# Kernel tuning notes

Measured on AMD Instinct MI355X. Metric: run time of the kernel, lower is better.

The kernel has to match this reference:

```python
import jax, jax.numpy as jnp
import numpy as np

B, S, D = 8, 1024, 1024
H = 16
D_HEAD = D // H
RANK = 256
NC = 64
NE = 64
KC = 16  # top_k_compress
KE = 8   # top_k_expand


def setup_inputs() -> dict:
    key = jax.random.key(0)
    ks = jax.random.split(key, 9)
    rn = lambda k, sh, s=1.0: jax.random.normal(k, sh, jnp.float32) * s
    return {
        "x": rn(ks[0], (B, S, D)),
        "importance": jax.random.uniform(ks[1], (B, S), jnp.float32),
        "W_compress": rn(ks[2], (NC, D), 1.0 / np.sqrt(D)),
        "W_Q": rn(ks[3], (NE, D), 1.0 / np.sqrt(D)),
        "W_K": rn(ks[4], (NE, D), 1.0 / np.sqrt(D)),
        "W_V": rn(ks[5], (NE, D), 1.0 / np.sqrt(D)),
        "compress_neurons": rn(ks[6], (NC, D, RANK), 1.0 / np.sqrt(D)),
        "expand_pool": rn(ks[7], (NE, RANK, D), 1.0 / np.sqrt(RANK)),
        "W_O": rn(ks[8], (D, D), 1.0 / np.sqrt(D)),
    }


def _route(x, importance, W, k):
    """Per-token softmax router, importance-aggregated, top-k renormalized."""
    pref = jax.nn.softmax(jnp.einsum('bsd,nd->bsn', x, W), axis=-1)  # [B,S,n]
    w = jnp.einsum('bs,bsn->bn', importance, pref)                   # [B,n]
    w = w / (w.sum(-1, keepdims=True) + 1e-8)
    tw, ti = jax.lax.top_k(w, k)                                     # [B,k]
    tw = tw / (tw.sum(-1, keepdims=True) + 1e-8)
    return tw, ti


def reference(x, importance, W_compress, W_Q, W_K, W_V, compress_neurons, expand_pool, W_O):
    # --- GlobalRouters.get_attention_weights ---
    cw, ci = _route(x, importance, W_compress, KC)
    qw, qi = _route(x, importance, W_Q, KE)
    kw, ki = _route(x, importance, W_K, KE)
    vw, vi = _route(x, importance, W_V, KE)

    # --- NeuronCircuit.forward ---
    # gather + mix compress neurons: [B,KC,D,R] -> [B,D,R]
    shared_c = jnp.einsum('bk,bkdr->bdr', cw, compress_neurons[ci])
    h = jnp.einsum('bsd,bdr->bsr', x, shared_c)  # [B,S,R]

    eQ = jnp.einsum('bk,bkrd->brd', qw, expand_pool[qi])
    eK = jnp.einsum('bk,bkrd->brd', kw, expand_pool[ki])
    eV = jnp.einsum('bk,bkrd->brd', vw, expand_pool[vi])

    def heads(t):  # [B,S,D] -> [B,H,S,d_head]
        return t.reshape(B, S, H, D_HEAD).transpose(0, 2, 1, 3)

    Q = heads(jnp.einsum('bsr,brd->bsd', h, eQ))
    K = heads(jnp.einsum('bsr,brd->bsd', h, eK))
    V = heads(jnp.einsum('bsr,brd->bsd', h, eV))

    scale = 1.0 / np.sqrt(D_HEAD)
    scores = jnp.einsum('bhqd,bhkd->bhqk', Q, K) * scale
    causal = jnp.tril(jnp.ones((S, S), dtype=bool))
    scores = jnp.where(causal, scores, jnp.finfo(scores.dtype).min)
    attn = jax.nn.softmax(scores, axis=-1)
    out = jnp.einsum('bhqk,bhkd->bhqd', attn, V)
    out = out.transpose(0, 2, 1, 3).reshape(B, S, D)
    return jnp.einsum('bsd,ed->bse', out, W_O)  # expand_O (Linear, no bias)
```

## Files before the change

kernel.cpp:

```cpp
#include <hip/hip_runtime.h>

typedef __attribute__((ext_vector_type(8))) short short8;
typedef __attribute__((ext_vector_type(4))) short short4v;
typedef __attribute__((ext_vector_type(4))) float f32x4;
typedef unsigned short u16;
typedef unsigned int u32;

__device__ __forceinline__ float bf2f(u16 h) {
    return __uint_as_float(((u32)h) << 16);
}
__device__ __forceinline__ u16 f2bf(float f) {
    u32 u = __float_as_uint(f);
    u32 r = u + 0x7fffu + ((u >> 16) & 1u);
    return (u16)(r >> 16);
}
__device__ __forceinline__ u32 pack_bf(float a, float b) {
    return __builtin_amdgcn_perm(__float_as_uint(b), __float_as_uint(a), 0x07060302u);
}

__device__ __forceinline__ void async_copy16(const void* g, void* l) {
    __builtin_amdgcn_global_load_lds(
        (const __attribute__((address_space(1))) void*)g,
        (__attribute__((address_space(3))) void*)l, 16, 0, 0);
}

__global__ __launch_bounds__(256) void cvt_split(
    const float* __restrict__ in, u16* __restrict__ hi, u16* __restrict__ lo, int n4)
{
    int i = blockIdx.x * 256 + threadIdx.x;
    if (i >= n4) return;
    float4 v = ((const float4*)in)[i];
    short4v h, l;
    float vv[4] = {v.x, v.y, v.z, v.w};
#pragma unroll
    for (int j = 0; j < 4; j++) {
        u16 hb = f2bf(vv[j]);
        h[j] = (short)hb;
        l[j] = (short)f2bf(vv[j] - bf2f(hb));
    }
    ((short4v*)hi)[i] = h;
    ((short4v*)lo)[i] = l;
}

__global__ __launch_bounds__(256) void cvt_split_w4(
    const float* __restrict__ w0, const float* __restrict__ w1,
    const float* __restrict__ w2, const float* __restrict__ w3,
    u16* __restrict__ hi, u16* __restrict__ lo)
{
    const int r = blockIdx.x >> 6;
    const float* src = (r == 0) ? w0 : (r == 1) ? w1 : (r == 2) ? w2 : w3;
    int i = (blockIdx.x & 63) * 256 + threadIdx.x;
    float4 v = ((const float4*)src)[i];
    short4v h, l;
    float vv[4] = {v.x, v.y, v.z, v.w};
#pragma unroll
    for (int j = 0; j < 4; j++) {
        u16 hb = f2bf(vv[j]);
        h[j] = (short)hb;
        l[j] = (short)f2bf(vv[j] - bf2f(hb));
    }
    ((short4v*)(hi + (long)r * 65536))[i] = h;
    ((short4v*)(lo + (long)r * 65536))[i] = l;
}

__global__ __launch_bounds__(256) void cvt_bf(
    const float* __restrict__ in, u16* __restrict__ out, int n4)
{
    int i = blockIdx.x * 256 + threadIdx.x;
    if (i >= n4) return;
    float4 v = ((const float4*)in)[i];
    short4v h;
    h[0] = (short)f2bf(v.x); h[1] = (short)f2bf(v.y);
    h[2] = (short)f2bf(v.z); h[3] = (short)f2bf(v.w);
    ((short4v*)out)[i] = h;
}

template <typename CT>
__global__ __launch_bounds__(256) void gemm_bt(
    const u16* __restrict__ A, long lda, long bsA,
    const u16* __restrict__ Bm, long ldb, long bsB,
    CT* __restrict__ C, long ldc, long bsC, int K, float cscale)
{
    __shared__ __align__(16) u16 lsA[128 * 32];
    __shared__ __align__(16) u16 lsB[128 * 32];
    const int tid = threadIdx.x;
    const int wave = tid >> 6, lane = tid & 63;
    const int quad = lane >> 4, l15 = lane & 15;
    const int wm = wave >> 1, wn = wave & 1;
    const long m0 = (long)blockIdx.x * 128, n0 = (long)blockIdx.y * 128;
    A  += (long)blockIdx.z * bsA;
    Bm += (long)blockIdx.z * bsB;
    C  += (long)blockIdx.z * bsC;
    const int srow = lane >> 2, scol = (lane & 3) * 8;

    f32x4 acc[4][4];
#pragma unroll
    for (int i = 0; i < 4; i++)
#pragma unroll
        for (int j = 0; j < 4; j++) acc[i][j] = (f32x4){0.f, 0.f, 0.f, 0.f};

    const u16* ga0 = A + (m0 + (wave * 2 + 0) * 16 + srow) * lda + scol;
    const u16* ga1 = A + (m0 + (wave * 2 + 1) * 16 + srow) * lda + scol;
    const u16* gb0 = Bm + (n0 + (wave * 2 + 0) * 16 + srow) * ldb + scol;
    const u16* gb1 = Bm + (n0 + (wave * 2 + 1) * 16 + srow) * ldb + scol;
    u16* la0 = &lsA[(wave * 2 + 0) * 512];
    u16* la1 = &lsA[(wave * 2 + 1) * 512];
    u16* lb0 = &lsB[(wave * 2 + 0) * 512];
    u16* lb1 = &lsB[(wave * 2 + 1) * 512];

    for (int kk = 0; kk < K; kk += 32) {
        async_copy16(ga0 + kk, la0);
        async_copy16(ga1 + kk, la1);
        async_copy16(gb0 + kk, lb0);
        async_copy16(gb1 + kk, lb1);
        __syncthreads();
        short8 af[4], bf[4];
#pragma unroll
        for (int mt = 0; mt < 4; mt++)
            af[mt] = *(const short8*)&lsA[(wm * 64 + mt * 16 + l15) * 32 + quad * 8];
#pragma unroll
        for (int nt = 0; nt < 4; nt++)
            bf[nt] = *(const short8*)&lsB[(wn * 64 + nt * 16 + l15) * 32 + quad * 8];
#pragma unroll
        for (int mt = 0; mt < 4; mt++)
#pragma unroll
            for (int nt = 0; nt < 4; nt++)
                acc[mt][nt] = __builtin_amdgcn_mfma_f32_16x16x32_bf16(
                    af[mt], bf[nt], acc[mt][nt], 0, 0, 0);
        __syncthreads();
    }
#pragma unroll
    for (int mt = 0; mt < 4; mt++) {
        const long rowb = m0 + wm * 64 + mt * 16 + quad * 4;
#pragma unroll
        for (int nt = 0; nt < 4; nt++) {
            const long col = n0 + wn * 64 + nt * 16 + l15;
#pragma unroll
            for (int r = 0; r < 4; r++) {
                const float v = acc[mt][nt][r] * cscale;
                if constexpr (sizeof(CT) == 2)
                    C[(rowb + r) * ldc + col] = f2bf(v);
                else
                    C[(rowb + r) * ldc + col] = v;
            }
        }
    }
}

__global__ __launch_bounds__(256) void gemm_router(
    const u16* __restrict__ Ah, const u16* __restrict__ Al,
    const u16* __restrict__ Bh, const u16* __restrict__ Bl,
    float* __restrict__ C)
{
    __shared__ __align__(16) u16 lsA[128 * 32];
    __shared__ __align__(16) u16 lsB[128 * 32];
    const int tid = threadIdx.x;
    const int wave = tid >> 6, lane = tid & 63;
    const int quad = lane >> 4, l15 = lane & 15;
    const int wm = wave >> 1, wn = wave & 1;
    const long m0 = (long)blockIdx.x * 128, n0 = (long)blockIdx.y * 128;
    const int srow = lane >> 2, scol = (lane & 3) * 8;
    const long offA = (m0 + (wave * 2) * 16 + srow) * 1024 + scol;
    const long offB = (n0 + (wave * 2) * 16 + srow) * 1024 + scol;
    u16* la0 = &lsA[(wave * 2 + 0) * 512];
    u16* la1 = &lsA[(wave * 2 + 1) * 512];
    u16* lb0 = &lsB[(wave * 2 + 0) * 512];
    u16* lb1 = &lsB[(wave * 2 + 1) * 512];

    f32x4 acc[4][4];
#pragma unroll
    for (int i = 0; i < 4; i++)
#pragma unroll
        for (int j = 0; j < 4; j++) acc[i][j] = (f32x4){0.f, 0.f, 0.f, 0.f};

    for (int seg = 0; seg < 3; seg++) {
        const u16* A = (seg == 1) ? Al : Ah;
        const u16* B = (seg == 2) ? Bl : Bh;
        const u16* ga = A + offA;
        const u16* gb = B + offB;
        for (int kk = 0; kk < 1024; kk += 32) {
            async_copy16(ga + kk, la0);
            async_copy16(ga + 16384 + kk, la1);
            async_copy16(gb + kk, lb0);
            async_copy16(gb + 16384 + kk, lb1);
            __syncthreads();
            short8 af[4], bf[4];
#pragma unroll
            for (int mt = 0; mt < 4; mt++)
                af[mt] = *(const short8*)&lsA[(wm * 64 + mt * 16 + l15) * 32 + quad * 8];
#pragma unroll
            for (int nt = 0; nt < 4; nt++)
                bf[nt] = *(const short8*)&lsB[(wn * 64 + nt * 16 + l15) * 32 + quad * 8];
#pragma unroll
            for (int mt = 0; mt < 4; mt++)
#pragma unroll
                for (int nt = 0; nt < 4; nt++)
                    acc[mt][nt] = __builtin_amdgcn_mfma_f32_16x16x32_bf16(
                        af[mt], bf[nt], acc[mt][nt], 0, 0, 0);
            __syncthreads();
        }
    }
#pragma unroll
    for (int mt = 0; mt < 4; mt++) {
        const long rowb = m0 + wm * 64 + mt * 16 + quad * 4;
#pragma unroll
        for (int nt = 0; nt < 4; nt++) {
            const long col = n0 + wn * 64 + nt * 16 + l15;
#pragma unroll
            for (int r = 0; r < 4; r++)
                C[(rowb + r) * 256 + col] = acc[mt][nt][r];
        }
    }
}

__global__ __launch_bounds__(128) void router_agg(
    const float* __restrict__ logits, const float* __restrict__ imp,
    float* __restrict__ w_raw)
{
    __shared__ float pref[32][257];
    const int tid = threadIdx.x;
    const int tl = tid >> 2, r = tid & 3;
    const int s = blockIdx.x * 32 + tl;
    const int b = s >> 10;
    const float* lp = logits + (long)s * 256 + r * 64;
    float v[64];
#pragma unroll
    for (int i = 0; i < 16; i++) {
        float4 f = ((const float4*)lp)[i];
        v[i * 4 + 0] = f.x; v[i * 4 + 1] = f.y;
        v[i * 4 + 2] = f.z; v[i * 4 + 3] = f.w;
    }
    float mx = v[0];
#pragma unroll
    for (int i = 1; i < 64; i++) mx = fmaxf(mx, v[i]);
    float sum = 0.f;
#pragma unroll
    for (int i = 0; i < 64; i++) { v[i] = __expf(v[i] - mx); sum += v[i]; }
    const float scale = imp[s] / sum;
#pragma unroll
    for (int i = 0; i < 64; i++) pref[tl][r * 64 + i] = v[i] * scale;
    __syncthreads();
#pragma unroll
    for (int half = 0; half < 2; half++) {
        const int idx = tid + half * 128;
        const int r2 = idx >> 6, n = idx & 63;
        float acc = 0.f;
#pragma unroll 8
        for (int t = 0; t < 32; t++) acc += pref[t][r2 * 64 + n];
        atomicAdd(&w_raw[(r2 * 8 + b) * 64 + n], acc);
    }
}

__global__ void topk_kernel(const float* __restrict__ w_raw,
                            float* __restrict__ topw, int* __restrict__ topi)
{
    const int r = blockIdx.x >> 3, b = blockIdx.x & 7;
    const int lane = threadIdx.x;
    const int k = (r == 0) ? 16 : 8;
    float w = w_raw[(r * 8 + b) * 64 + lane];
    float tot = w;
    for (int o2 = 32; o2 >= 1; o2 >>= 1) tot += __shfl_xor(tot, o2);
    w = w / (tot + 1e-8f);
    __shared__ float tw[16];
    __shared__ int ti[16];
    float cur = w;
    float ssum = 0.f;
    for (int j = 0; j < k; j++) {
        float m = cur; int mi = lane;
        for (int o2 = 32; o2 >= 1; o2 >>= 1) {
            float om = __shfl_xor(m, o2); int oi = __shfl_xor(mi, o2);
            if (om > m || (om == m && oi < mi)) { m = om; mi = oi; }
        }
        if (lane == 0) { tw[j] = m; ti[j] = mi; }
        ssum += m;
        if (lane == mi) cur = -1e30f;
    }
    __syncthreads();
    if (lane < 16) {
        topw[(r * 8 + b) * 16 + lane] = (lane < k) ? tw[lane] / (ssum + 1e-8f) : 0.f;
        topi[(r * 8 + b) * 16 + lane] = (lane < k) ? ti[lane] : 0;
    }
}

__global__ __launch_bounds__(256) void gather_mix(
    const float* __restrict__ pool, const float* __restrict__ topw,
    const int* __restrict__ topi, u16* __restrict__ out,
    int I, int J, int k)
{
    __shared__ float tile[64][65];
    const int b = blockIdx.z;
    const long IJ = (long)I * J;
    const int i0 = blockIdx.x * 64, j0 = blockIdx.y * 64;
    const float* tw = topw + b * 16;
    const int* ti = topi + b * 16;
    const int tid = threadIdx.x;
    const int il = tid >> 2, jg = tid & 3;
    float acc[16];
#pragma unroll
    for (int m = 0; m < 16; m++) acc[m] = 0.f;
    for (int kk = 0; kk < k; kk++) {
        const float wgt = tw[kk];
        const long n = ti[kk];
        const float* src = pool + n * IJ + (long)(i0 + il) * J + j0 + jg * 16;
        float4 a0 = ((const float4*)src)[0];
        float4 a1 = ((const float4*)src)[1];
        float4 a2 = ((const float4*)src)[2];
        float4 a3 = ((const float4*)src)[3];
        acc[0] += wgt * a0.x;  acc[1] += wgt * a0.y;
        acc[2] += wgt * a0.z;  acc[3] += wgt * a0.w;
        acc[4] += wgt * a1.x;  acc[5] += wgt * a1.y;
        acc[6] += wgt * a1.z;  acc[7] += wgt * a1.w;
        acc[8] += wgt * a2.x;  acc[9] += wgt * a2.y;
        acc[10] += wgt * a2.z; acc[11] += wgt * a2.w;
        acc[12] += wgt * a3.x; acc[13] += wgt * a3.y;
        acc[14] += wgt * a3.z; acc[15] += wgt * a3.w;
    }
#pragma unroll
    for (int m = 0; m < 16; m++) tile[il][jg * 16 + m] = acc[m];
    __syncthreads();
    const int jl = tid >> 2, ig = tid & 3;
    short8 o0, o1;
#pragma unroll
    for (int m = 0; m < 8; m++) {
        o0[m] = (short)f2bf(tile[ig * 16 + m][jl]);
        o1[m] = (short)f2bf(tile[ig * 16 + 8 + m][jl]);
    }
    u16* dst = out + (long)b * IJ + (long)(j0 + jl) * I + i0 + ig * 16;
    *(short8*)dst = o0;
    *(short8*)(dst + 8) = o1;
}

__global__ __launch_bounds__(256, 2) void flash_attn(
    const u16* __restrict__ Qg, const u16* __restrict__ Kg,
    const u16* __restrict__ Vt, u16* __restrict__ Og)
{
    __shared__ __align__(16) u16 plds[4][32 * 72];
    const int tid = threadIdx.x;
    const int wv = tid >> 6, lane = tid & 63;
    const int quad = lane >> 4, l15 = lane & 15;
    const int gw = blockIdx.x * 4 + wv;
    const int pr = gw & 15;
    const int bh = gw >> 4;
    const int hh = bh & 15, bb = bh >> 4;
    const long SD = 1024L * 1024L;
    const u16* Qb = Qg + (long)bb * SD + hh * 64;
    const u16* Kb = Kg + (long)bb * SD + hh * 64;
    const u16* Vb = Vt + (long)bb * SD + (long)hh * 64 * 1024;
    u16* myp = plds[wv];

    for (int half = 0; half < 2; half++) {
        const int qt = half ? (31 - pr) : pr;
        const int q0 = qt * 32;

        short8 qf[2][2];
#pragma unroll
        for (int mt = 0; mt < 2; mt++)
#pragma unroll
            for (int kb = 0; kb < 2; kb++)
                qf[mt][kb] = *(const short8*)(Qb + (long)(q0 + mt * 16 + l15) * 1024 + kb * 32 + quad * 8);

        f32x4 o[2][4];
        float mrow[2] = {-3e38f, -3e38f}, lrow[2] = {0.f, 0.f};
#pragma unroll
        for (int mt = 0; mt < 2; mt++)
#pragma unroll
            for (int nt = 0; nt < 4; nt++) o[mt][nt] = (f32x4){0.f, 0.f, 0.f, 0.f};

        const int ntile = (q0 + 95) >> 6;
        short8 kf[4][2], kn[4][2];
#pragma unroll
        for (int kt = 0; kt < 4; kt++)
#pragma unroll
            for (int kb = 0; kb < 2; kb++)
                kf[kt][kb] = *(const short8*)(Kb + (long)(kt * 16 + l15) * 1024 + kb * 32 + quad * 8);

        for (int it = 0; it < ntile; it++) {
            const int k2 = it * 64;
            const bool last = (it == ntile - 1);
            f32x4 st[4][2];
#pragma unroll
            for (int kt = 0; kt < 4; kt++)
#pragma unroll
                for (int q_ = 0; q_ < 2; q_++) {
                    f32x4 z = (f32x4){0.f, 0.f, 0.f, 0.f};
                    z = __builtin_amdgcn_mfma_f32_16x16x32_bf16(kf[kt][0], qf[q_][0], z, 0, 0, 0);
                    z = __builtin_amdgcn_mfma_f32_16x16x32_bf16(kf[kt][1], qf[q_][1], z, 0, 0, 0);
                    st[kt][q_] = z;
                }
            short8 vf[4][2];
#pragma unroll
            for (int nt = 0; nt < 4; nt++)
#pragma unroll
                for (int kh = 0; kh < 2; kh++)
                    vf[nt][kh] = *(const short8*)(Vb + (long)(nt * 16 + l15) * 1024 + k2 + kh * 32 + quad * 8);
            if (it + 1 < ntile) {
#pragma unroll
                for (int kt = 0; kt < 4; kt++)
#pragma unroll
                    for (int kb = 0; kb < 2; kb++)
                        kn[kt][kb] = *(const short8*)(Kb + (long)(k2 + 64 + kt * 16 + l15) * 1024 + kb * 32 + quad * 8);
            }
            float am[2];
#pragma unroll
            for (int q_ = 0; q_ < 2; q_++) {
                if (last) {
#pragma unroll
                    for (int kt = 0; kt < 4; kt++)
#pragma unroll
                        for (int r = 0; r < 4; r++)
                            if (k2 + kt * 16 + quad * 4 + r > q0 + q_ * 16 + l15)
                                st[kt][q_][r] = -3e38f;
                }
                float cm = -3e38f;
#pragma unroll
                for (int kt = 0; kt < 4; kt++)
#pragma unroll
                    for (int r = 0; r < 4; r++) cm = fmaxf(cm, st[kt][q_][r]);
                cm = fmaxf(cm, __shfl_xor(cm, 16));
                cm = fmaxf(cm, __shfl_xor(cm, 32));
                const float mn = fmaxf(mrow[q_], cm);
                am[q_] = exp2f(mrow[q_] - mn);
                mrow[q_] = mn;
                const float moff = 0.00281502f - mn;
                float rs = 0.f;
#pragma unroll
                for (int kt = 0; kt < 4; kt++) {
                    float p0 = exp2f(st[kt][q_][0] + moff);
                    float p1 = exp2f(st[kt][q_][1] + moff);
                    float p2 = exp2f(st[kt][q_][2] + moff);
                    float p3 = exp2f(st[kt][q_][3] + moff);
                    rs += (p0 + p1) + (p2 + p3);
                    u32 w0 = pack_bf(p0, p1);
                    u32 w1 = pack_bf(p2, p3);
                    *(uint2*)&myp[(q_ * 16 + l15) * 72 + kt * 16 + quad * 4] = make_uint2(w0, w1);
                }
                rs += __shfl_xor(rs, 16);
                rs += __shfl_xor(rs, 32);
                lrow[q_] = lrow[q_] * am[q_] + rs;
            }
            float av[2][4];
#pragma unroll
            for (int mt = 0; mt < 2; mt++)
#pragma unroll
                for (int r = 0; r < 4; r++)
                    av[mt][r] = __shfl(am[mt], quad * 4 + r);
            asm volatile("s_waitcnt lgkmcnt(0)" ::: "memory");
            short8 pf0[2], pf1[2];
#pragma unroll
            for (int kh = 0; kh < 2; kh++) {
                pf0[kh] = *(const short8*)&myp[(l15) * 72 + kh * 32 + quad * 8];
                pf1[kh] = *(const short8*)&myp[(16 + l15) * 72 + kh * 32 + quad * 8];
            }
#pragma unroll
            for (int mt = 0; mt < 2; mt++)
#pragma unroll
                for (int nt = 0; nt < 4; nt++)
#pragma unroll
                    for (int r = 0; r < 4; r++) o[mt][nt][r] *= av[mt][r];
#pragma unroll
            for (int nt = 0; nt < 4; nt++)
#pragma unroll
                for (int kh = 0; kh < 2; kh++) {
                    o[0][nt] = __builtin_amdgcn_mfma_f32_16x16x32_bf16(pf0[kh], vf[nt][kh], o[0][nt], 0, 0, 0);
                    o[1][nt] = __builtin_amdgcn_mfma_f32_16x16x32_bf16(pf1[kh], vf[nt][kh], o[1][nt], 0, 0, 0);
                }
            if (it + 1 < ntile) {
#pragma unroll
                for (int kt = 0; kt < 4; kt++)
#pragma unroll
                    for (int kb = 0; kb < 2; kb++) kf[kt][kb] = kn[kt][kb];
            }
        }
#pragma unroll
        for (int mt = 0; mt < 2; mt++)
#pragma unroll
            for (int r = 0; r < 4; r++) {
                const float li = 1.0f / __shfl(lrow[mt], quad * 4 + r);
                const long row = q0 + mt * 16 + quad * 4 + r;
#pragma unroll
                for (int nt = 0; nt < 4; nt++)
                    Og[(long)bb * SD + row * 1024 + hh * 64 + nt * 16 + l15] =
                        f2bf(o[mt][nt][r] * li);
            }
    }
}

extern "C" void kernel_launch(void* const* d_in, const int* in_sizes, int n_in,
                              void* d_out, int out_size, void* d_ws, size_t ws_size,
                              hipStream_t stream)
{
    const float* x   = (const float*)d_in[0];
    const float* imp = (const float*)d_in[1];
    const float* cn  = (const float*)d_in[6];
    const float* ep  = (const float*)d_in[7];
    const float* Wo  = (const float*)d_in[8];
    float* outp = (float*)d_out;
    char* ws = (char*)d_ws;

    u16* xh = (u16*)d_out;
    u16* xl = xh + 8388608;

    u16*   Wh     = (u16*)(ws + 0);
    u16*   Wl     = (u16*)(ws + 524288);
    u16*   Wobf   = (u16*)(ws + 1048576);
    float* w_raw  = (float*)(ws + 3145728);
    float* topw   = (float*)(ws + 3153920);
    int*   topi   = (int*)(ws + 3155968);
    float* logits = (float*)(ws + 4194304);
    u16*   scT    = (u16*)(ws + 12582912);
    u16*   eQT    = (u16*)(ws + 16777216);
    u16*   Kb     = (u16*)(ws + 4194304);
    u16*   hbuf   = (u16*)(ws + 20971520);
    u16*   eKT    = (u16*)(ws + 25165824);
    u16*   eVT    = (u16*)(ws + 29360128);
    u16*   Qb     = (u16*)(ws + 33554432);
    u16*   VTb    = (u16*)(ws + 50331648);
    u16*   aout   = (u16*)(ws + 67108864);

    cvt_split<<<dim3(8192), 256, 0, stream>>>(x, xh, xl, 2097152);
    cvt_split_w4<<<dim3(256), 256, 0, stream>>>(
        (const float*)d_in[2], (const float*)d_in[3],
        (const float*)d_in[4], (const float*)d_in[5], Wh, Wl);
    cvt_bf<<<dim3(1024), 256, 0, stream>>>(Wo, Wobf, 262144);
    hipMemsetAsync(w_raw, 0, 4 * 8 * 64 * 4, stream);

    gemm_router<<<dim3(64, 2, 1), 256, 0, stream>>>(xh, xl, Wh, Wl, logits);
    router_agg<<<dim3(256), 128, 0, stream>>>(logits, imp, w_raw);
    topk_kernel<<<dim3(32), 64, 0, stream>>>(w_raw, topw, topi);
    gather_mix<<<dim3(16, 4, 8), 256, 0, stream>>>(cn, topw + 0 * 128, topi + 0 * 128, scT, 1024, 256, 16);
    gather_mix<<<dim3(4, 16, 8), 256, 0, stream>>>(ep, topw + 1 * 128, topi + 1 * 128, eQT, 256, 1024, 8);
    gather_mix<<<dim3(4, 16, 8), 256, 0, stream>>>(ep, topw + 2 * 128, topi + 2 * 128, eKT, 256, 1024, 8);
    gather_mix<<<dim3(4, 16, 8), 256, 0, stream>>>(ep, topw + 3 * 128, topi + 3 * 128, eVT, 256, 1024, 8);
    gemm_bt<u16><<<dim3(8, 2, 8), 256, 0, stream>>>(
        xh, 1024, 1048576, scT, 1024, 262144, hbuf, 256, 262144, 1024, 1.0f);
    gemm_bt<u16><<<dim3(8, 8, 8), 256, 0, stream>>>(
        hbuf, 256, 262144, eQT, 256, 262144, Qb, 1024, 1048576, 256, 0.180336880111f);
    gemm_bt<u16><<<dim3(8, 8, 8), 256, 0, stream>>>(
        hbuf, 256, 262144, eKT, 256, 262144, Kb, 1024, 1048576, 256, 1.0f);
    gemm_bt<u16><<<dim3(8, 8, 8), 256, 0, stream>>>(
        eVT, 256, 262144, hbuf, 256, 262144, VTb, 1024, 1048576, 256, 1.0f);
    flash_attn<<<dim3(512), 256, 0, stream>>>(Qb, Kb, VTb, aout);
    gemm_bt<float><<<dim3(64, 8, 1), 256, 0, stream>>>(
        aout, 1024, 0, Wobf, 1024, 0, outp, 1024, 0, 1024, 1.0f);
}
```

Measured before the change: 448.8 us.

## Split-K router and h GEMMs, batch QKV launches, shrink flash-attn tiles

The router GEMM and the x·compress GEMM are split along K, with partial results combined through float atomics into zeroed buffers. This is meant to fill more CUs, since the original grids were small. The three expand gathers and the three Q/K/V GEMMs are each merged into a single launch via blockIdx.z. Flash attention now handles 16-row query tiles per wave with no K prefetch, giving twice the blocks and a higher occupancy bound. The cost is extra memsets, atomic traffic, a separate fp32-to-bf16 conversion pass for h, and nondeterministic summation order.

```diff
diff --git a/kernel.cpp b/kernel.cpp
--- a/kernel.cpp
+++ b/kernel.cpp
@@ -147,58 +147,63 @@
     }
 }
 
-__global__ __launch_bounds__(256) void gemm_router(
-    const u16* __restrict__ Ah, const u16* __restrict__ Al,
-    const u16* __restrict__ Bh, const u16* __restrict__ Bl,
-    float* __restrict__ C)
+__global__ __launch_bounds__(256) void gemm_qkv(
+    const u16* __restrict__ hbuf, const u16* __restrict__ eQT,
+    const u16* __restrict__ eKT, const u16* __restrict__ eVT,
+    u16* __restrict__ Qb, u16* __restrict__ Kb, u16* __restrict__ VTb,
+    float qscale)
 {
     __shared__ __align__(16) u16 lsA[128 * 32];
     __shared__ __align__(16) u16 lsB[128 * 32];
+    const int mode = blockIdx.z >> 3, b = blockIdx.z & 7;
+    const long off256 = (long)b * 262144, off1k = (long)b * 1048576;
+    const u16* A  = (mode == 2) ? (eVT + off256) : (hbuf + off256);
+    const u16* Bm = (mode == 0) ? (eQT + off256) : (mode == 1) ? (eKT + off256) : (hbuf + off256);
+    u16* C = ((mode == 0) ? Qb : (mode == 1) ? Kb : VTb) + off1k;
+    const float cscale = (mode == 0) ? qscale : 1.0f;
+
     const int tid = threadIdx.x;
     const int wave = tid >> 6, lane = tid & 63;
     const int quad = lane >> 4, l15 = lane & 15;
     const int wm = wave >> 1, wn = wave & 1;
     const long m0 = (long)blockIdx.x * 128, n0 = (long)blockIdx.y * 128;
     const int srow = lane >> 2, scol = (lane & 3) * 8;
-    const long offA = (m0 + (wave * 2) * 16 + srow) * 1024 + scol;
-    const long offB = (n0 + (wave * 2) * 16 + srow) * 1024 + scol;
+
+    f32x4 acc[4][4];
+#pragma unroll
+    for (int i = 0; i < 4; i++)
+#pragma unroll
+        for (int j = 0; j < 4; j++) acc[i][j] = (f32x4){0.f, 0.f, 0.f, 0.f};
+
+    const u16* ga0 = A + (m0 + (wave * 2 + 0) * 16 + srow) * 256 + scol;
+    const u16* ga1 = A + (m0 + (wave * 2 + 1) * 16 + srow) * 256 + scol;
+    const u16* gb0 = Bm + (n0 + (wave * 2 + 0) * 16 + srow) * 256 + scol;
+    const u16* gb1 = Bm + (n0 + (wave * 2 + 1) * 16 + srow) * 256 + scol;
     u16* la0 = &lsA[(wave * 2 + 0) * 512];
     u16* la1 = &lsA[(wave * 2 + 1) * 512];
     u16* lb0 = &lsB[(wave * 2 + 0) * 512];
     u16* lb1 = &lsB[(wave * 2 + 1) * 512];
 
-    f32x4 acc[4][4];
-#pragma unroll
-    for (int i = 0; i < 4; i++)
-#pragma unroll
-        for (int j = 0; j < 4; j++) acc[i][j] = (f32x4){0.f, 0.f, 0.f, 0.f};
-
-    for (int seg = 0; seg < 3; seg++) {
-        const u16* A = (seg == 1) ? Al : Ah;
-        const u16* B = (seg == 2) ? Bl : Bh;
-        const u16* ga = A + offA;
-        const u16* gb = B + offB;
-        for (int kk = 0; kk < 1024; kk += 32) {
-            async_copy16(ga + kk, la0);
-            async_copy16(ga + 16384 + kk, la1);
-            async_copy16(gb + kk, lb0);
-            async_copy16(gb + 16384 + kk, lb1);
-            __syncthreads();
-            short8 af[4], bf[4];
-#pragma unroll
-            for (int mt = 0; mt < 4; mt++)
-                af[mt] = *(const short8*)&lsA[(wm * 64 + mt * 16 + l15) * 32 + quad * 8];
+    for (int kk = 0; kk < 256; kk += 32) {
+        async_copy16(ga0 + kk, la0);
+        async_copy16(ga1 + kk, la1);
+        async_copy16(gb0 + kk, lb0);
+        async_copy16(gb1 + kk, lb1);
+        __syncthreads();
+        short8 af[4], bf[4];
+#pragma unroll
+        for (int mt = 0; mt < 4; mt++)
+            af[mt] = *(const short8*)&lsA[(wm * 64 + mt * 16 + l15) * 32 + quad * 8];
+#pragma unroll
+        for (int nt = 0; nt < 4; nt++)
+            bf[nt] = *(const short8*)&lsB[(wn * 64 + nt * 16 + l15) * 32 + quad * 8];
+#pragma unroll
+        for (int mt = 0; mt < 4; mt++)
 #pragma unroll
             for (int nt = 0; nt < 4; nt++)
-                bf[nt] = *(const short8*)&lsB[(wn * 64 + nt * 16 + l15) * 32 + quad * 8];
-#pragma unroll
-            for (int mt = 0; mt < 4; mt++)
-#pragma unroll
-                for (int nt = 0; nt < 4; nt++)
-                    acc[mt][nt] = __builtin_amdgcn_mfma_f32_16x16x32_bf16(
-                        af[mt], bf[nt], acc[mt][nt], 0, 0, 0);
-            __syncthreads();
-        }
+                acc[mt][nt] = __builtin_amdgcn_mfma_f32_16x16x32_bf16(
+                    af[mt], bf[nt], acc[mt][nt], 0, 0, 0);
+        __syncthreads();
     }
 #pragma unroll
     for (int mt = 0; mt < 4; mt++) {
@@ -208,7 +213,134 @@
             const long col = n0 + wn * 64 + nt * 16 + l15;
 #pragma unroll
             for (int r = 0; r < 4; r++)
-                C[(rowb + r) * 256 + col] = acc[mt][nt][r];
+                C[(rowb + r) * 1024 + col] = f2bf(acc[mt][nt][r] * cscale);
+        }
+    }
+}
+
+__global__ __launch_bounds__(256) void gemm_router(
+    const u16* __restrict__ Ah, const u16* __restrict__ Al,
+    const u16* __restrict__ Bh, const u16* __restrict__ Bl,
+    float* __restrict__ C)
+{
+    __shared__ __align__(16) u16 lsA[128 * 32];
+    __shared__ __align__(16) u16 lsB[128 * 32];
+    const int seg = blockIdx.z >> 1;
+    const int kk0 = (blockIdx.z & 1) * 512;
+    const u16* A = (seg == 1) ? Al : Ah;
+    const u16* B = (seg == 2) ? Bl : Bh;
+    const int tid = threadIdx.x;
+    const int wave = tid >> 6, lane = tid & 63;
+    const int quad = lane >> 4, l15 = lane & 15;
+    const int wm = wave >> 1, wn = wave & 1;
+    const long m0 = (long)blockIdx.x * 128, n0 = (long)blockIdx.y * 128;
+    const int srow = lane >> 2, scol = (lane & 3) * 8;
+    const u16* ga = A + (m0 + (wave * 2) * 16 + srow) * 1024 + scol + kk0;
+    const u16* gb = B + (n0 + (wave * 2) * 16 + srow) * 1024 + scol + kk0;
+    u16* la0 = &lsA[(wave * 2 + 0) * 512];
+    u16* la1 = &lsA[(wave * 2 + 1) * 512];
+    u16* lb0 = &lsB[(wave * 2 + 0) * 512];
+    u16* lb1 = &lsB[(wave * 2 + 1) * 512];
+
+    f32x4 acc[4][4];
+#pragma unroll
+    for (int i = 0; i < 4; i++)
+#pragma unroll
+        for (int j = 0; j < 4; j++) acc[i][j] = (f32x4){0.f, 0.f, 0.f, 0.f};
+
+    for (int kk = 0; kk < 512; kk += 32) {
+        async_copy16(ga + kk, la0);
+        async_copy16(ga + 16384 + kk, la1);
+        async_copy16(gb + kk, lb0);
+        async_copy16(gb + 16384 + kk, lb1);
+        __syncthreads();
+        short8 af[4], bf[4];
+#pragma unroll
+        for (int mt = 0; mt < 4; mt++)
+            af[mt] = *(const short8*)&lsA[(wm * 64 + mt * 16 + l15) * 32 + quad * 8];
+#pragma unroll
+        for (int nt = 0; nt < 4; nt++)
+            bf[nt] = *(const short8*)&lsB[(wn * 64 + nt * 16 + l15) * 32 + quad * 8];
+#pragma unroll
+        for (int mt = 0; mt < 4; mt++)
+#pragma unroll
+            for (int nt = 0; nt < 4; nt++)
+                acc[mt][nt] = __builtin_amdgcn_mfma_f32_16x16x32_bf16(
+                    af[mt], bf[nt], acc[mt][nt], 0, 0, 0);
+        __syncthreads();
+    }
+#pragma unroll
+    for (int mt = 0; mt < 4; mt++) {
+        const long rowb = m0 + wm * 64 + mt * 16 + quad * 4;
+#pragma unroll
+        for (int nt = 0; nt < 4; nt++) {
+            const long col = n0 + wn * 64 + nt * 16 + l15;
+#pragma unroll
+            for (int r = 0; r < 4; r++)
+                atomicAdd(&C[(rowb + r) * 256 + col], acc[mt][nt][r]);
+        }
+    }
+}
+
+__global__ __launch_bounds__(256) void gemm_h(
+    const u16* __restrict__ xh, const u16* __restrict__ scT, float* __restrict__ hf)
+{
+    __shared__ __align__(16) u16 lsA[128 * 32];
+    __shared__ __align__(16) u16 lsB[128 * 32];
+    const int b = blockIdx.z >> 1;
+    const int kk0 = (blockIdx.z & 1) * 512;
+    const u16* A = xh + (long)b * 1048576;
+    const u16* Bm = scT + (long)b * 262144;
+    float* C = hf + (long)b * 262144;
+    const int tid = threadIdx.x;
+    const int wave = tid >> 6, lane = tid & 63;
+    const int quad = lane >> 4, l15 = lane & 15;
+    const int wm = wave >> 1, wn = wave & 1;
+    const long m0 = (long)blockIdx.x * 128, n0 = (long)blockIdx.y * 128;
+    const int srow = lane >> 2, scol = (lane & 3) * 8;
+    const u16* ga = A + (m0 + (wave * 2) * 16 + srow) * 1024 + scol + kk0;
+    const u16* gb = Bm + (n0 + (wave * 2) * 16 + srow) * 1024 + scol + kk0;
+    u16* la0 = &lsA[(wave * 2 + 0) * 512];
+    u16* la1 = &lsA[(wave * 2 + 1) * 512];
+    u16* lb0 = &lsB[(wave * 2 + 0) * 512];
+    u16* lb1 = &lsB[(wave * 2 + 1) * 512];
+
+    f32x4 acc[4][4];
+#pragma unroll
+    for (int i = 0; i < 4; i++)
+#pragma unroll
+        for (int j = 0; j < 4; j++) acc[i][j] = (f32x4){0.f, 0.f, 0.f, 0.f};
+
+    for (int kk = 0; kk < 512; kk += 32) {
+        async_copy16(ga + kk, la0);
+        async_copy16(ga + 16384 + kk, la1);
+        async_copy16(gb + kk, lb0);
+        async_copy16(gb + 16384 + kk, lb1);
+        __syncthreads();
+        short8 af[4], bf[4];
+#pragma unroll
+        for (int mt = 0; mt < 4; mt++)
+            af[mt] = *(const short8*)&lsA[(wm * 64 + mt * 16 + l15) * 32 + quad * 8];
+#pragma unroll
+        for (int nt = 0; nt < 4; nt++)
+            bf[nt] = *(const short8*)&lsB[(wn * 64 + nt * 16 + l15) * 32 + quad * 8];
+#pragma unroll
+        for (int mt = 0; mt < 4; mt++)
+#pragma unroll
+            for (int nt = 0; nt < 4; nt++)
+                acc[mt][nt] = __builtin_amdgcn_mfma_f32_16x16x32_bf16(
+                    af[mt], bf[nt], acc[mt][nt], 0, 0, 0);
+        __syncthreads();
+    }
+#pragma unroll
+    for (int mt = 0; mt < 4; mt++) {
+        const long rowb = m0 + wm * 64 + mt * 16 + quad * 4;
+#pragma unroll
+        for (int nt = 0; nt < 4; nt++) {
+            const long col = n0 + wn * 64 + nt * 16 + l15;
+#pragma unroll
+            for (int r = 0; r < 4; r++)
+                atomicAdd(&C[(rowb + r) * 256 + col], acc[mt][nt][r]);
         }
     }
 }
@@ -330,17 +462,66 @@
     *(short8*)(dst + 8) = o1;
 }
 
-__global__ __launch_bounds__(256, 2) void flash_attn(
+__global__ __launch_bounds__(256) void gather_mix_e3(
+    const float* __restrict__ pool, const float* __restrict__ topw,
+    const int* __restrict__ topi,
+    u16* __restrict__ oQ, u16* __restrict__ oK, u16* __restrict__ oV)
+{
+    __shared__ float tile[64][65];
+    const int rr = blockIdx.z >> 3, b = blockIdx.z & 7;
+    u16* out = (rr == 0) ? oQ : (rr == 1) ? oK : oV;
+    const float* tw = topw + (rr + 1) * 128 + b * 16;
+    const int* ti = topi + (rr + 1) * 128 + b * 16;
+    const long IJ = 256L * 1024L;
+    const int i0 = blockIdx.x * 64, j0 = blockIdx.y * 64;
+    const int tid = threadIdx.x;
+    const int il = tid >> 2, jg = tid & 3;
+    float acc[16];
+#pragma unroll
+    for (int m = 0; m < 16; m++) acc[m] = 0.f;
+    for (int kk = 0; kk < 8; kk++) {
+        const float wgt = tw[kk];
+        const long n = ti[kk];
+        const float* src = pool + n * IJ + (long)(i0 + il) * 1024 + j0 + jg * 16;
+        float4 a0 = ((const float4*)src)[0];
+        float4 a1 = ((const float4*)src)[1];
+        float4 a2 = ((const float4*)src)[2];
+        float4 a3 = ((const float4*)src)[3];
+        acc[0] += wgt * a0.x;  acc[1] += wgt * a0.y;
+        acc[2] += wgt * a0.z;  acc[3] += wgt * a0.w;
+        acc[4] += wgt * a1.x;  acc[5] += wgt * a1.y;
+        acc[6] += wgt * a1.z;  acc[7] += wgt * a1.w;
+        acc[8] += wgt * a2.x;  acc[9] += wgt * a2.y;
+        acc[10] += wgt * a2.z; acc[11] += wgt * a2.w;
+        acc[12] += wgt * a3.x; acc[13] += wgt * a3.y;
+        acc[14] += wgt * a3.z; acc[15] += wgt * a3.w;
+    }
+#pragma unroll
+    for (int m = 0; m < 16; m++) tile[il][jg * 16 + m] = acc[m];
+    __syncthreads();
+    const int jl = tid >> 2, ig = tid & 3;
+    short8 o0, o1;
+#pragma unroll
+    for (int m = 0; m < 8; m++) {
+        o0[m] = (short)f2bf(tile[ig * 16 + m][jl]);
+        o1[m] = (short)f2bf(tile[ig * 16 + 8 + m][jl]);
+    }
+    u16* dst = out + (long)b * IJ + (long)(j0 + jl) * 256 + i0 + ig * 16;
+    *(short8*)dst = o0;
+    *(short8*)(dst + 8) = o1;
+}
+
+__global__ __launch_bounds__(256, 4) void flash_attn(
     const u16* __restrict__ Qg, const u16* __restrict__ Kg,
     const u16* __restrict__ Vt, u16* __restrict__ Og)
 {
-    __shared__ __align__(16) u16 plds[4][32 * 72];
+    __shared__ __align__(16) u16 plds[4][16 * 72];
     const int tid = threadIdx.x;
     const int wv = tid >> 6, lane = tid & 63;
     const int quad = lane >> 4, l15 = lane & 15;
     const int gw = blockIdx.x * 4 + wv;
-    const int pr = gw & 15;
-    const int bh = gw >> 4;
+    const int pr = gw & 31;
+    const int bh = gw >> 5;
     const int hh = bh & 15, bb = bh >> 4;
     const long SD = 1024L * 1024L;
     const u16* Qb = Qg + (long)bb * SD + hh * 64;
@@ -349,139 +530,98 @@
     u16* myp = plds[wv];
 
     for (int half = 0; half < 2; half++) {
-        const int qt = half ? (31 - pr) : pr;
-        const int q0 = qt * 32;
-
-        short8 qf[2][2];
-#pragma unroll
-        for (int mt = 0; mt < 2; mt++)
-#pragma unroll
-            for (int kb = 0; kb < 2; kb++)
-                qf[mt][kb] = *(const short8*)(Qb + (long)(q0 + mt * 16 + l15) * 1024 + kb * 32 + quad * 8);
-
-        f32x4 o[2][4];
-        float mrow[2] = {-3e38f, -3e38f}, lrow[2] = {0.f, 0.f};
-#pragma unroll
-        for (int mt = 0; mt < 2; mt++)
-#pragma unroll
-            for (int nt = 0; nt < 4; nt++) o[mt][nt] = (f32x4){0.f, 0.f, 0.f, 0.f};
-
-        const int ntile = (q0 + 95) >> 6;
-        short8 kf[4][2], kn[4][2];
-#pragma unroll
-        for (int kt = 0; kt < 4; kt++)
-#pragma unroll
-            for (int kb = 0; kb < 2; kb++)
-                kf[kt][kb] = *(const short8*)(Kb + (long)(kt * 16 + l15) * 1024 + kb * 32 + quad * 8);
-
+        const int qt = half ? (63 - pr) : pr;
+        const int q0 = qt * 16;
+
+        short8 qf[2];
+#pragma unroll
+        for (int kb = 0; kb < 2; kb++)
+            qf[kb] = *(const short8*)(Qb + (long)(q0 + l15) * 1024 + kb * 32 + quad * 8);
+
+        f32x4 o[4];
+        float mrow = -3e38f, lrow = 0.f;
+#pragma unroll
+        for (int nt = 0; nt < 4; nt++) o[nt] = (f32x4){0.f, 0.f, 0.f, 0.f};
+
+        const int ntile = (q0 + 79) >> 6;
         for (int it = 0; it < ntile; it++) {
             const int k2 = it * 64;
             const bool last = (it == ntile - 1);
-            f32x4 st[4][2];
-#pragma unroll
-            for (int kt = 0; kt < 4; kt++)
-#pragma unroll
-                for (int q_ = 0; q_ < 2; q_++) {
-                    f32x4 z = (f32x4){0.f, 0.f, 0.f, 0.f};
-                    z = __builtin_amdgcn_mfma_f32_16x16x32_bf16(kf[kt][0], qf[q_][0], z, 0, 0, 0);
-                    z = __builtin_amdgcn_mfma_f32_16x16x32_bf16(kf[kt][1], qf[q_][1], z, 0, 0, 0);
-                    st[kt][q_] = z;
-                }
+            f32x4 st[4];
+#pragma unroll
+            for (int kt = 0; kt < 4; kt++) {
+                short8 kf0 = *(const short8*)(Kb + (long)(k2 + kt * 16 + l15) * 1024 + quad * 8);
+                short8 kf1 = *(const short8*)(Kb + (long)(k2 + kt * 16 + l15) * 1024 + 32 + quad * 8);
+                f32x4 z = (f32x4){0.f, 0.f, 0.f, 0.f};
+                z = __builtin_amdgcn_mfma_f32_16x16x32_bf16(kf0, qf[0], z, 0, 0, 0);
+                z = __builtin_amdgcn_mfma_f32_16x16x32_bf16(kf1, qf[1], z, 0, 0, 0);
+                st[kt] = z;
+            }
             short8 vf[4][2];
 #pragma unroll
             for (int nt = 0; nt < 4; nt++)
 #pragma unroll
                 for (int kh = 0; kh < 2; kh++)
                     vf[nt][kh] = *(const short8*)(Vb + (long)(nt * 16 + l15) * 1024 + k2 + kh * 32 + quad * 8);
-            if (it + 1 < ntile) {
+            if (last) {
 #pragma unroll
                 for (int kt = 0; kt < 4; kt++)
 #pragma unroll
-                    for (int kb = 0; kb < 2; kb++)
-                        kn[kt][kb] = *(const short8*)(Kb + (long)(k2 + 64 + kt * 16 + l15) * 1024 + kb * 32 + quad * 8);
+                    for (int r = 0; r < 4; r++)
+                        if (k2 + kt * 16 + quad * 4 + r > q0 + l15)
+                            st[kt][r] = -3e38f;
             }
-            float am[2];
-#pragma unroll
-            for (int q_ = 0; q_ < 2; q_++) {
-                if (last) {
-#pragma unroll
-                    for (int kt = 0; kt < 4; kt++)
-#pragma unroll
-                        for (int r = 0; r < 4; r++)
-                            if (k2 + kt * 16 + quad * 4 + r > q0 + q_ * 16 + l15)
-                                st[kt][q_][r] = -3e38f;
-                }
-                float cm = -3e38f;
-#pragma unroll
-                for (int kt = 0; kt < 4; kt++)
-#pragma unroll
-                    for (int r = 0; r < 4; r++) cm = fmaxf(cm, st[kt][q_][r]);
-                cm = fmaxf(cm, __shfl_xor(cm, 16));
-                cm = fmaxf(cm, __shfl_xor(cm, 32));
-                const float mn = fmaxf(mrow[q_], cm);
-                am[q_] = exp2f(mrow[q_] - mn);
-                mrow[q_] = mn;
-                const float moff = 0.00281502f - mn;
-                float rs = 0.f;
-#pragma unroll
-                for (int kt = 0; kt < 4; kt++) {
-                    float p0 = exp2f(st[kt][q_][0] + moff);
-                    float p1 = exp2f(st[kt][q_][1] + moff);
-                    float p2 = exp2f(st[kt][q_][2] + moff);
-                    float p3 = exp2f(st[kt][q_][3] + moff);
-                    rs += (p0 + p1) + (p2 + p3);
-                    u32 w0 = pack_bf(p0, p1);
-                    u32 w1 = pack_bf(p2, p3);
-                    *(uint2*)&myp[(q_ * 16 + l15) * 72 + kt * 16 + quad * 4] = make_uint2(w0, w1);
-                }
-                rs += __shfl_xor(rs, 16);
-                rs += __shfl_xor(rs, 32);
-                lrow[q_] = lrow[q_] * am[q_] + rs;
+            float cm = -3e38f;
+#pragma unroll
+            for (int kt = 0; kt < 4; kt++)
+#pragma unroll
+                for (int r = 0; r < 4; r++) cm = fmaxf(cm, st[kt][r]);
+            cm = fmaxf(cm, __shfl_xor(cm, 16));
+            cm = fmaxf(cm, __shfl_xor(cm, 32));
+            const float mn = fmaxf(mrow, cm);
+            const float am = exp2f(mrow - mn);
+            mrow = mn;
+            const float moff = 0.00281502f - mn;
+            float rs = 0.f;
+#pragma unroll
+            for (int kt = 0; kt < 4; kt++) {
+                float p0 = exp2f(st[kt][0] + moff);
+                float p1 = exp2f(st[kt][1] + moff);
+                float p2 = exp2f(st[kt][2] + moff);
+                float p3 = exp2f(st[kt][3] + moff);
+                rs += (p0 + p1) + (p2 + p3);
+                *(uint2*)&myp[l15 * 72 + kt * 16 + quad * 4] =
+                    make_uint2(pack_bf(p0, p1), pack_bf(p2, p3));
             }
-            float av[2][4];
-#pragma unroll
-            for (int mt = 0; mt < 2; mt++)
-#pragma unroll
-                for (int r = 0; r < 4; r++)
-                    av[mt][r] = __shfl(am[mt], quad * 4 + r);
+            rs += __shfl_xor(rs, 16);
+            rs += __shfl_xor(rs, 32);
+            lrow = lrow * am + rs;
+            float av[4];
+#pragma unroll
+            for (int r = 0; r < 4; r++) av[r] = __shfl(am, quad * 4 + r);
             asm volatile("s_waitcnt lgkmcnt(0)" ::: "memory");
-            short8 pf0[2], pf1[2];
-#pragma unroll
-            for (int kh = 0; kh < 2; kh++) {
-                pf0[kh] = *(const short8*)&myp[(l15) * 72 + kh * 32 + quad * 8];
-                pf1[kh] = *(const short8*)&myp[(16 + l15) * 72 + kh * 32 + quad * 8];
-            }
-#pragma unroll
-            for (int mt = 0; mt < 2; mt++)
-#pragma unroll
-                for (int nt = 0; nt < 4; nt++)
-#pragma unroll
-                    for (int r = 0; r < 4; r++) o[mt][nt][r] *= av[mt][r];
-#pragma unroll
-            for (int nt = 0; nt < 4; nt++)
-#pragma unroll
-                for (int kh = 0; kh < 2; kh++) {
-                    o[0][nt] = __builtin_amdgcn_mfma_f32_16x16x32_bf16(pf0[kh], vf[nt][kh], o[0][nt], 0, 0, 0);
-                    o[1][nt] = __builtin_amdgcn_mfma_f32_16x16x32_bf16(pf1[kh], vf[nt][kh], o[1][nt], 0, 0, 0);
-                }
-            if (it + 1 < ntile) {
-#pragma unroll
-                for (int kt = 0; kt < 4; kt++)
-#pragma unroll
-                    for (int kb = 0; kb < 2; kb++) kf[kt][kb] = kn[kt][kb];
+            short8 pf[2];
+#pragma unroll
+            for (int kh = 0; kh < 2; kh++)
+                pf[kh] = *(const short8*)&myp[l15 * 72 + kh * 32 + quad * 8];
+#pragma unroll
+            for (int nt = 0; nt < 4; nt++) {
+#pragma unroll
+                for (int r = 0; r < 4; r++) o[nt][r] *= av[r];
+#pragma unroll
+                for (int kh = 0; kh < 2; kh++)
+                    o[nt] = __builtin_amdgcn_mfma_f32_16x16x32_bf16(pf[kh], vf[nt][kh], o[nt], 0, 0, 0);
             }
         }
 #pragma unroll
-        for (int mt = 0; mt < 2; mt++)
-#pragma unroll
-            for (int r = 0; r < 4; r++) {
-                const float li = 1.0f / __shfl(lrow[mt], quad * 4 + r);
-                const long row = q0 + mt * 16 + quad * 4 + r;
-#pragma unroll
-                for (int nt = 0; nt < 4; nt++)
-                    Og[(long)bb * SD + row * 1024 + hh * 64 + nt * 16 + l15] =
-                        f2bf(o[mt][nt][r] * li);
-            }
+        for (int r = 0; r < 4; r++) {
+            const float li = 1.0f / __shfl(lrow, quad * 4 + r);
+            const long row = q0 + quad * 4 + r;
+#pragma unroll
+            for (int nt = 0; nt < 4; nt++)
+                Og[(long)bb * SD + row * 1024 + hh * 64 + nt * 16 + l15] =
+                    f2bf(o[nt][r] * li);
+        }
     }
 }
 
@@ -507,15 +647,16 @@
     float* topw   = (float*)(ws + 3153920);
     int*   topi   = (int*)(ws + 3155968);
     float* logits = (float*)(ws + 4194304);
+    float* hf32   = (float*)(ws + 4194304);
     u16*   scT    = (u16*)(ws + 12582912);
-    u16*   eQT    = (u16*)(ws + 16777216);
-    u16*   Kb     = (u16*)(ws + 4194304);
-    u16*   hbuf   = (u16*)(ws + 20971520);
+    u16*   hbuf   = (u16*)(ws + 16777216);
+    u16*   eQT    = (u16*)(ws + 20971520);
     u16*   eKT    = (u16*)(ws + 25165824);
     u16*   eVT    = (u16*)(ws + 29360128);
     u16*   Qb     = (u16*)(ws + 33554432);
-    u16*   VTb    = (u16*)(ws + 50331648);
-    u16*   aout   = (u16*)(ws + 67108864);
+    u16*   Kb     = (u16*)(ws + 50331648);
+    u16*   VTb    = (u16*)(ws + 67108864);
+    u16*   aout   = (u16*)(ws + 4194304);
 
     cvt_split<<<dim3(8192), 256, 0, stream>>>(x, xh, xl, 2097152);
     cvt_split_w4<<<dim3(256), 256, 0, stream>>>(
@@ -523,23 +664,19 @@
         (const float*)d_in[4], (const float*)d_in[5], Wh, Wl);
     cvt_bf<<<dim3(1024), 256, 0, stream>>>(Wo, Wobf, 262144);
     hipMemsetAsync(w_raw, 0, 4 * 8 * 64 * 4, stream);
-
-    gemm_router<<<dim3(64, 2, 1), 256, 0, stream>>>(xh, xl, Wh, Wl, logits);
+    hipMemsetAsync(logits, 0, 8388608, stream);
+
+    gemm_router<<<dim3(64, 2, 6), 256, 0, stream>>>(xh, xl, Wh, Wl, logits);
     router_agg<<<dim3(256), 128, 0, stream>>>(logits, imp, w_raw);
     topk_kernel<<<dim3(32), 64, 0, stream>>>(w_raw, topw, topi);
-    gather_mix<<<dim3(16, 4, 8), 256, 0, stream>>>(cn, topw + 0 * 128, topi + 0 * 128, scT, 1024, 256, 16);
-    gather_mix<<<dim3(4, 16, 8), 256, 0, stream>>>(ep, topw + 1 * 128, topi + 1 * 128, eQT, 256, 1024, 8);
-    gather_mix<<<dim3(4, 16, 8), 256, 0, stream>>>(ep, topw + 2 * 128, topi + 2 * 128, eKT, 256, 1024, 8);
-    gather_mix<<<dim3(4, 16, 8), 256, 0, stream>>>(ep, topw + 3 * 128, topi + 3 * 128, eVT, 256, 1024, 8);
-    gemm_bt<u16><<<dim3(8, 2, 8), 256, 0, stream>>>(
-        xh, 1024, 1048576, scT, 1024, 262144, hbuf, 256, 262144, 1024, 1.0f);
-    gemm_bt<u16><<<dim3(8, 8, 8), 256, 0, stream>>>(
-        hbuf, 256, 262144, eQT, 256, 262144, Qb, 1024, 1048576, 256, 0.180336880111f);
-    gemm_bt<u16><<<dim3(8, 8, 8), 256, 0, stream>>>(
-        hbuf, 256, 262144, eKT, 256, 262144, Kb, 1024, 1048576, 256, 1.0f);
-    gemm_bt<u16><<<dim3(8, 8, 8), 256, 0, stream>>>(
-        eVT, 256, 262144, hbuf, 256, 262144, VTb, 1024, 1048576, 256, 1.0f);
-    flash_attn<<<dim3(512), 256, 0, stream>>>(Qb, Kb, VTb, aout);
+    hipMemsetAsync(hf32, 0, 8388608, stream);
+    gather_mix<<<dim3(16, 4, 8), 256, 0, stream>>>(cn, topw, topi, scT, 1024, 256, 16);
+    gather_mix_e3<<<dim3(4, 16, 24), 256, 0, stream>>>(ep, topw, topi, eQT, eKT, eVT);
+    gemm_h<<<dim3(8, 2, 16), 256, 0, stream>>>(xh, scT, hf32);
+    cvt_bf<<<dim3(2048), 256, 0, stream>>>(hf32, hbuf, 524288);
+    gemm_qkv<<<dim3(8, 8, 24), 256, 0, stream>>>(
+        hbuf, eQT, eKT, eVT, Qb, Kb, VTb, 0.180336880111f);
+    flash_attn<<<dim3(1024), 256, 0, stream>>>(Qb, Kb, VTb, aout);
     gemm_bt<float><<<dim3(64, 8, 1), 256, 0, stream>>>(
         aout, 1024, 0, Wobf, 1024, 0, outp, 1024, 0, 1024, 1.0f);
 }
```

New measurement: 514.9 us. 14.7% more time.
